# Performance work log

Measured on AMD Instinct MI355X. Metric: run time of the kernel, lower is better.

The kernel has to match this reference:

```python
import jax, jax.numpy as jnp
import numpy as np

NUM_KERNELS = 5


def setup_inputs() -> dict:
    key = jax.random.key(0)
    k1, k2 = jax.random.split(key)
    B, D = 4096, 256
    return {
        "s_feat": jax.random.normal(k1, (B, D), dtype=jnp.float32),
        "t_feat": jax.random.normal(k2, (B, D), dtype=jnp.float32),
    }


def _pairwise_sq_dists(feats):
    # Gram-matrix form of sum((x_i - x_j)**2, axis=-1); same math as the
    # broadcasted (x - y)**2 sum, without the [N, N, D] intermediate.
    sq = jnp.sum(feats * feats, axis=-1)  # [N]
    d = sq[:, None] + sq[None, :] - 2.0 * (feats @ feats.T)  # [N, N]
    return jnp.maximum(d, 0.0)


def reference(s_feat, t_feat):
    batch = s_feat.shape[0]
    feats = jnp.concatenate((s_feat, t_feat), axis=0)  # [2B, D]
    distances = _pairwise_sq_dists(feats)  # [2B, 2B]

    # Median-heuristic-style bandwidth (detached in original).
    n = 2 * batch
    bandwidth = float(n * n - n) / jnp.sum(jax.lax.stop_gradient(distances))
    bandwidth = bandwidth / (2 ** (NUM_KERNELS // 2))
    gammas = [bandwidth * (2 ** i) for i in range(NUM_KERNELS)]

    # Multi-gamma Gaussian kernel average (fixed small loop over kernels).
    kern = sum(jnp.exp(-distances * g) for g in gammas) / NUM_KERNELS

    s2s = kern[:batch, :batch]
    t2t = kern[batch:, batch:]
    s2t = kern[:batch, batch:]
    disc = jnp.mean(s2s + t2t - 2.0 * s2t)
    return disc
```

## Files before the change

kernel.cpp:

```cpp
#include <hip/hip_runtime.h>
#include <stdint.h>
#include <math.h>

#define BATCH 4096
#define NT    8192
#define FD    256
#define TM    256
#define TN    128
#define BK    32
#define NUMK  5
#define NBLK  1056
#define PBLK  1024

typedef __attribute__((ext_vector_type(8))) short bf16x8;
typedef __attribute__((ext_vector_type(4))) float f32x4;

static const size_t WS_FB    = 0;
static const size_t WS_SQ    = (size_t)NT * FD * 2;
static const size_t WS_PCOL  = WS_SQ + (size_t)NT * 4;
static const size_t WS_WSUM  = WS_PCOL + (size_t)PBLK * 256 * 4;
static const size_t WS_GAMMA = WS_WSUM + (size_t)PBLK * 4;

__device__ __forceinline__ unsigned short f2bf_rne(float x) {
    unsigned u = __float_as_uint(x);
    unsigned r = (u + 0x7fffu + ((u >> 16) & 1u)) >> 16;
    return (unsigned short)r;
}

__device__ __forceinline__ void async_copy16(void* lds, const void* g) {
    __builtin_amdgcn_global_load_lds(
        (__attribute__((address_space(1))) void*)(void*)(const_cast<void*>(g)),
        (__attribute__((address_space(3))) void*)lds, 16, 0, 0);
}

__global__ void mmd_prep(const float* __restrict__ s_feat,
                         const float* __restrict__ t_feat,
                         unsigned short* __restrict__ fb,
                         float* __restrict__ sq,
                         float* __restrict__ pcol,
                         float* __restrict__ wsum) {
    __shared__ float cp[4][FD];
    __shared__ float rw[4];
    const int w    = threadIdx.x >> 6;
    const int lane = threadIdx.x & 63;
    float c0 = 0.f, c1 = 0.f, c2 = 0.f, c3 = 0.f;
    float wtot = 0.f;
#pragma unroll
    for (int t = 0; t < 2; ++t) {
        int row = blockIdx.x * 8 + w * 2 + t;
        const float* src = (row < BATCH) ? (s_feat + (size_t)row * FD)
                                         : (t_feat + (size_t)(row - BATCH) * FD);
        float4 v = ((const float4*)src)[lane];
        unsigned int u01 = (unsigned)f2bf_rne(v.x) | ((unsigned)f2bf_rne(v.y) << 16);
        unsigned int u23 = (unsigned)f2bf_rne(v.z) | ((unsigned)f2bf_rne(v.w) << 16);
        ((uint2*)(fb + (size_t)row * FD))[lane] = make_uint2(u01, u23);
        float ss = v.x * v.x + v.y * v.y + v.z * v.z + v.w * v.w;
        for (int off = 32; off; off >>= 1) ss += __shfl_down(ss, off);
        if (lane == 0) { sq[row] = ss; wtot += ss; }
        c0 += v.x; c1 += v.y; c2 += v.z; c3 += v.w;
    }
    cp[w][4 * lane + 0] = c0;
    cp[w][4 * lane + 1] = c1;
    cp[w][4 * lane + 2] = c2;
    cp[w][4 * lane + 3] = c3;
    if (lane == 0) rw[w] = wtot;
    __syncthreads();
    int t = threadIdx.x;
    pcol[(size_t)blockIdx.x * 256 + t] = cp[0][t] + cp[1][t] + cp[2][t] + cp[3][t];
    if (t == 0) wsum[blockIdx.x] = rw[0] + rw[1] + rw[2] + rw[3];
}

__global__ void mmd_gamma(const float* __restrict__ pcol,
                          const float* __restrict__ wsum,
                          float* __restrict__ gamma,
                          float* __restrict__ out) {
    __shared__ float gcol[4][256];
    __shared__ float redc[4], redw[16];
    const int tid  = threadIdx.x;
    const int c    = tid & 255, s = tid >> 8;
    const int lane = tid & 63;
    float a0 = 0.f, a1 = 0.f, a2 = 0.f, a3 = 0.f;
#pragma unroll 4
    for (int k = 0; k < 256; k += 4) {
        a0 += pcol[(size_t)(s * 256 + k + 0) * 256 + c];
        a1 += pcol[(size_t)(s * 256 + k + 1) * 256 + c];
        a2 += pcol[(size_t)(s * 256 + k + 2) * 256 + c];
        a3 += pcol[(size_t)(s * 256 + k + 3) * 256 + c];
    }
    gcol[s][c] = (a0 + a1) + (a2 + a3);
    float wv = wsum[tid];
    for (int off = 32; off; off >>= 1) wv += __shfl_down(wv, off);
    if (lane == 0) redw[tid >> 6] = wv;
    __syncthreads();
    if (tid < 256) {
        float colv = gcol[0][c] + gcol[1][c] + gcol[2][c] + gcol[3][c];
        float cv2 = colv * colv;
        for (int off = 32; off; off >>= 1) cv2 += __shfl_down(cv2, off);
        if (lane == 0) redc[tid >> 6] = cv2;
    }
    __syncthreads();
    if (tid == 0) {
        float s2 = (redc[0] + redc[1]) + (redc[2] + redc[3]);
        float ssq = 0.f;
#pragma unroll
        for (int i = 0; i < 16; ++i) ssq += redw[i];
        float sumd = 2.0f * (float)NT * ssq - 2.0f * s2;
        float n2n  = (float)((long long)NT * NT - NT);
        gamma[0]   = 0.25f * (n2n / sumd);
        out[0]     = 0.f;
    }
}

__global__ __launch_bounds__(512, 4) void mmd_main(
    const unsigned short* __restrict__ fb,
    const float* __restrict__ sq,
    const float* __restrict__ gamma,
    float* __restrict__ out) {
    const int bid = blockIdx.x;
    const int swz = (bid & 7) * (NBLK / 8) + (bid >> 3);
    int I = (int)((65.0f - sqrtf(fmaxf(4225.0f - 4.0f * (float)swz, 0.f))) * 0.5f);
    if (I > 31) I = 31;
    while (I > 0 && I * (65 - I) > swz) --I;
    while (I < 31 && (I + 1) * (65 - (I + 1)) <= swz) ++I;
    const int J = 2 * I + (swz - I * (65 - I));
    const bool straddle = ((J >> 1) == I);

    __shared__ __align__(16) unsigned short a_t[3][TM * BK];
    __shared__ __align__(16) unsigned short b_t[3][TN * BK];
    __shared__ float sqa[TM], sqb[TN];
    __shared__ float red[8];

    const int tid  = threadIdx.x;
    const int w    = tid >> 6, lane = tid & 63;
    const int wm2  = w >> 1, wn2 = w & 1;
    const int quad = lane >> 4, m16 = lane & 15;
    const int lrow16 = lane >> 2;
    const int pslot  = lane & 3;

    const size_t rowA0 = (size_t)I * TM;
    const size_t rowB0 = (size_t)J * TN;

    float sqv = 0.f;
    if (tid < TM)                sqv = sq[rowA0 + tid];
    else if (tid < TM + TN)      sqv = sq[rowB0 + (tid - TM)];
    const float g0 = gamma[0];

#define STAGE(buf, k0_) do {                                                   \
        _Pragma("unroll")                                                      \
        for (int q = 0; q < 2; ++q) {                                          \
            int rr_ = w * 32 + q * 16 + lrow16;                    \
            int gc_ = pslot ^ ((rr_ >> 1) & 3);                                \
            async_copy16(&a_t[buf][(w * 32 + q * 16) * BK],                    \
                         fb + (rowA0 + rr_) * FD + (k0_) + gc_ * 8);           \
        }                                                                      \
        {                                                                      \
            int rr_ = w * 16 + lrow16;                             \
            int gc_ = pslot ^ ((rr_ >> 1) & 3);                                \
            async_copy16(&b_t[buf][(w * 16) * BK],                             \
                         fb + (rowB0 + rr_) * FD + (k0_) + gc_ * 8);           \
        }                                                                      \
    } while (0)

    STAGE(0, 0);
    STAGE(1, BK);
    STAGE(2, 2 * BK);

    if (tid < TM)                sqa[tid] = sqv;
    else if (tid < TM + TN)      sqb[tid - TM] = sqv;

    const f32x4 fzero = {0.f, 0.f, 0.f, 0.f};
    f32x4 acc[4][4];
#pragma unroll
    for (int a = 0; a < 4; ++a)
#pragma unroll
        for (int b = 0; b < 4; ++b) acc[a][b] = fzero;

    __syncthreads();

#pragma unroll
    for (int st = 0; st < 8; ++st) {
        if (st > 0) {
            if (st >= 3) {
                if (st == 7) asm volatile("s_waitcnt vmcnt(0)" ::: "memory");
                else         asm volatile("s_waitcnt vmcnt(3)" ::: "memory");
            }
            __builtin_amdgcn_s_barrier();
            __builtin_amdgcn_sched_barrier(0);
            if (st <= 5) STAGE((st + 2) % 3, (st + 2) * BK);
        }
        const int cur = st % 3;

        bf16x8 af[4], bf[4];
#pragma unroll
        for (int tm = 0; tm < 4; ++tm) {
            int row = wm2 * 64 + tm * 16 + m16;
            int p = quad ^ ((row >> 1) & 3);
            af[tm] = *(const bf16x8*)&a_t[cur][row * BK + p * 8];
        }
#pragma unroll
        for (int tn = 0; tn < 4; ++tn) {
            int row = wn2 * 64 + tn * 16 + m16;
            int p = quad ^ ((row >> 1) & 3);
            bf[tn] = *(const bf16x8*)&b_t[cur][row * BK + p * 8];
        }
        __builtin_amdgcn_sched_barrier(0);

        __builtin_amdgcn_s_setprio(1);
#pragma unroll
        for (int tm = 0; tm < 4; ++tm)
#pragma unroll
            for (int tn = 0; tn < 4; ++tn)
                acc[tm][tn] = __builtin_amdgcn_mfma_f32_16x16x32_bf16(
                    af[tm], bf[tn], acc[tm][tn], 0, 0, 0);
        __builtin_amdgcn_s_setprio(0);
    }

    float ls[4] = {0.f, 0.f, 0.f, 0.f};
    if (!straddle) {
#pragma unroll
        for (int tm = 0; tm < 4; ++tm) {
            const int i0 = wm2 * 64 + tm * 16 + quad * 4;
            float sqi[4] = {sqa[i0 + 0], sqa[i0 + 1], sqa[i0 + 2], sqa[i0 + 3]};
#pragma unroll
            for (int tn = 0; tn < 4; ++tn) {
                const int j = wn2 * 64 + tn * 16 + m16;
                const float sqj = sqb[j];
#pragma unroll
                for (int rr = 0; rr < 4; ++rr) {
                    float d = fmaf(-2.f, acc[tm][tn][rr], sqi[rr] + sqj);
                    d = fmaxf(d, 0.f);
                    float e1 = __expf(-d * g0);
                    float e2 = e1 * e1, e4 = e2 * e2, e8 = e4 * e4, e16 = e8 * e8;
                    ls[rr] += e1 + e2 + e4 + e8 + e16;
                }
            }
        }
    } else {
        const int dOff = (J - 2 * I) * TN;
#pragma unroll
        for (int tm = 0; tm < 4; ++tm) {
            const int i0 = wm2 * 64 + tm * 16 + quad * 4;
            float sqi[4] = {sqa[i0 + 0], sqa[i0 + 1], sqa[i0 + 2], sqa[i0 + 3]};
#pragma unroll
            for (int tn = 0; tn < 4; ++tn) {
                const int j = wn2 * 64 + tn * 16 + m16;
                const float sqj = sqb[j];
                const int jg = j + dOff;
#pragma unroll
                for (int rr = 0; rr < 4; ++rr) {
                    const int ig = i0 + rr;
                    float wf = (jg > ig) ? 2.f : ((jg == ig) ? 1.f : 0.f);
                    float d = fmaf(-2.f, acc[tm][tn][rr], sqi[rr] + sqj);
                    d = fmaxf(d, 0.f);
                    float e1 = __expf(-d * g0);
                    float e2 = e1 * e1, e4 = e2 * e2, e8 = e4 * e4, e16 = e8 * e8;
                    ls[rr] += wf * (e1 + e2 + e4 + e8 + e16);
                }
            }
        }
    }
    float lsum = (ls[0] + ls[1]) + (ls[2] + ls[3]);
    for (int off = 32; off; off >>= 1) lsum += __shfl_down(lsum, off);
    if (lane == 0) red[w] = lsum;
    __syncthreads();
    if (tid == 0) {
        float wgt;
        if (straddle) wgt = 1.f;
        else wgt = ((I < 16) == (J < 32)) ? 2.f : -2.f;
        float scale = wgt * (1.f / NUMK) * (1.f / 16777216.f);
        float tot = ((red[0] + red[1]) + (red[2] + red[3]))
                  + ((red[4] + red[5]) + (red[6] + red[7]));
        atomicAdd(out, tot * scale);
    }
}

extern "C" void kernel_launch(void* const* d_in, const int* in_sizes, int n_in,
                              void* d_out, int out_size, void* d_ws, size_t ws_size,
                              hipStream_t stream) {
    const float* s_feat = (const float*)d_in[0];
    const float* t_feat = (const float*)d_in[1];
    char* ws = (char*)d_ws;
    unsigned short* fb = (unsigned short*)(ws + WS_FB);
    float* sq    = (float*)(ws + WS_SQ);
    float* pcol  = (float*)(ws + WS_PCOL);
    float* wsum  = (float*)(ws + WS_WSUM);
    float* gamma = (float*)(ws + WS_GAMMA);
    float* out   = (float*)d_out;

    mmd_prep<<<PBLK, 256, 0, stream>>>(s_feat, t_feat, fb, sq, pcol, wsum);
    mmd_gamma<<<1, 1024, 0, stream>>>(pcol, wsum, gamma, out);
    mmd_main<<<NBLK, 512, 0, stream>>>(fb, sq, gamma, out);
}
```

Before: 108.1 us.

## Use square 128x128 triangular tiles with per-wave private LDS double buffers

Replaces the 256x128 rectangular tiling over the triangle (with straddle-tile masking) with 2080 square 128x128 upper-triangular tiles, each handled by a 256-thread block of four waves. Every wave now loads its own 64-row A and B slices into a private LDS double buffer, which removes the block-wide barriers in the K loop. Diagonal tiles are weighted once and off-diagonal tiles twice, so the per-element masking goes away. In exchange, each wave fetches its own copies with no sharing of A/B across waves, so global/L2 traffic per tile goes up and occupancy changes.

```diff
diff --git a/kernel.cpp b/kernel.cpp
--- a/kernel.cpp
+++ b/kernel.cpp
@@ -5,11 +5,10 @@
 #define BATCH 4096
 #define NT    8192
 #define FD    256
-#define TM    256
-#define TN    128
+#define TILE  128
 #define BK    32
 #define NUMK  5
-#define NBLK  1056
+#define NTRI  2080
 #define PBLK  1024
 
 typedef __attribute__((ext_vector_type(8))) short bf16x8;
@@ -111,62 +110,61 @@
     }
 }
 
-__global__ __launch_bounds__(512, 4) void mmd_main(
+__global__ __launch_bounds__(256, 2) void mmd_main(
     const unsigned short* __restrict__ fb,
     const float* __restrict__ sq,
     const float* __restrict__ gamma,
     float* __restrict__ out) {
     const int bid = blockIdx.x;
-    const int swz = (bid & 7) * (NBLK / 8) + (bid >> 3);
-    int I = (int)((65.0f - sqrtf(fmaxf(4225.0f - 4.0f * (float)swz, 0.f))) * 0.5f);
-    if (I > 31) I = 31;
-    while (I > 0 && I * (65 - I) > swz) --I;
-    while (I < 31 && (I + 1) * (65 - (I + 1)) <= swz) ++I;
-    const int J = 2 * I + (swz - I * (65 - I));
-    const bool straddle = ((J >> 1) == I);
-
-    __shared__ __align__(16) unsigned short a_t[3][TM * BK];
-    __shared__ __align__(16) unsigned short b_t[3][TN * BK];
-    __shared__ float sqa[TM], sqb[TN];
-    __shared__ float red[8];
+    const int swz = (bid & 7) * (NTRI / 8) + (bid >> 3);
+    int r = (int)((sqrtf(8.0f * (float)swz + 1.0f) - 1.0f) * 0.5f);
+    while ((r + 1) * (r + 2) / 2 <= swz) ++r;
+    while (r * (r + 1) / 2 > swz) --r;
+    const int bi = swz - r * (r + 1) / 2;
+    const int bj = r;
+
+    __shared__ __align__(16) unsigned short a_t[4][2][64 * BK];
+    __shared__ __align__(16) unsigned short b_t[4][2][64 * BK];
+    __shared__ float sqa[TILE], sqb[TILE];
+    __shared__ float red[4];
 
     const int tid  = threadIdx.x;
     const int w    = tid >> 6, lane = tid & 63;
-    const int wm2  = w >> 1, wn2 = w & 1;
+    const int wm   = w >> 1, wn = w & 1;
     const int quad = lane >> 4, m16 = lane & 15;
     const int lrow16 = lane >> 2;
     const int pslot  = lane & 3;
 
-    const size_t rowA0 = (size_t)I * TM;
-    const size_t rowB0 = (size_t)J * TN;
+    const size_t rowA0 = (size_t)bi * TILE + wm * 64;
+    const size_t rowB0 = (size_t)bj * TILE + wn * 64;
 
     float sqv = 0.f;
-    if (tid < TM)                sqv = sq[rowA0 + tid];
-    else if (tid < TM + TN)      sqv = sq[rowB0 + (tid - TM)];
+    if (tid < TILE) sqv = sq[(size_t)bi * TILE + tid];
+    else            sqv = sq[(size_t)bj * TILE + (tid - TILE)];
     const float g0 = gamma[0];
 
-#define STAGE(buf, k0_) do {                                                   \
+#define STAGE_W(buf, k0_) do {                                                 \
         _Pragma("unroll")                                                      \
-        for (int q = 0; q < 2; ++q) {                                          \
-            int rr_ = w * 32 + q * 16 + lrow16;                    \
+        for (int q = 0; q < 4; ++q) {                                          \
+            int rr_ = q * 16 + lrow16;                    \
             int gc_ = pslot ^ ((rr_ >> 1) & 3);                                \
-            async_copy16(&a_t[buf][(w * 32 + q * 16) * BK],                    \
+            async_copy16(&a_t[w][buf][(q * 16) * BK],                          \
                          fb + (rowA0 + rr_) * FD + (k0_) + gc_ * 8);           \
         }                                                                      \
-        {                                                                      \
-            int rr_ = w * 16 + lrow16;                             \
+        _Pragma("unroll")                                                      \
+        for (int q = 0; q < 4; ++q) {                                          \
+            int rr_ = q * 16 + lrow16;                                         \
             int gc_ = pslot ^ ((rr_ >> 1) & 3);                                \
-            async_copy16(&b_t[buf][(w * 16) * BK],                             \
+            async_copy16(&b_t[w][buf][(q * 16) * BK],                          \
                          fb + (rowB0 + rr_) * FD + (k0_) + gc_ * 8);           \
         }                                                                      \
     } while (0)
 
-    STAGE(0, 0);
-    STAGE(1, BK);
-    STAGE(2, 2 * BK);
-
-    if (tid < TM)                sqa[tid] = sqv;
-    else if (tid < TM + TN)      sqb[tid - TM] = sqv;
+    STAGE_W(0, 0);
+    STAGE_W(1, BK);
+
+    if (tid < TILE) sqa[tid] = sqv;
+    else            sqb[tid - TILE] = sqv;
 
     const f32x4 fzero = {0.f, 0.f, 0.f, 0.f};
     f32x4 acc[4][4];
@@ -175,34 +173,29 @@
 #pragma unroll
         for (int b = 0; b < 4; ++b) acc[a][b] = fzero;
 
-    __syncthreads();
-
 #pragma unroll
     for (int st = 0; st < 8; ++st) {
-        if (st > 0) {
-            if (st >= 3) {
-                if (st == 7) asm volatile("s_waitcnt vmcnt(0)" ::: "memory");
-                else         asm volatile("s_waitcnt vmcnt(3)" ::: "memory");
-            }
-            __builtin_amdgcn_s_barrier();
-            __builtin_amdgcn_sched_barrier(0);
-            if (st <= 5) STAGE((st + 2) % 3, (st + 2) * BK);
+        const int cur = st & 1;
+        if (st == 7) asm volatile("s_waitcnt vmcnt(0)" ::: "memory");
+        else         asm volatile("s_waitcnt vmcnt(8)" ::: "memory");
+        __builtin_amdgcn_sched_barrier(0);
+
+        bf16x8 af[4], bf[4];
+#pragma unroll
+        for (int tm = 0; tm < 4; ++tm) {
+            int ra = tm * 16 + m16;
+            int p = quad ^ ((ra >> 1) & 3);
+            af[tm] = *(const bf16x8*)&a_t[w][cur][ra * BK + p * 8];
         }
-        const int cur = st % 3;
-
-        bf16x8 af[4], bf[4];
-#pragma unroll
-        for (int tm = 0; tm < 4; ++tm) {
-            int row = wm2 * 64 + tm * 16 + m16;
-            int p = quad ^ ((row >> 1) & 3);
-            af[tm] = *(const bf16x8*)&a_t[cur][row * BK + p * 8];
+#pragma unroll
+        for (int tn = 0; tn < 4; ++tn) {
+            int rb = tn * 16 + m16;
+            int p = quad ^ ((rb >> 1) & 3);
+            bf[tn] = *(const bf16x8*)&b_t[w][cur][rb * BK + p * 8];
         }
-#pragma unroll
-        for (int tn = 0; tn < 4; ++tn) {
-            int row = wn2 * 64 + tn * 16 + m16;
-            int p = quad ^ ((row >> 1) & 3);
-            bf[tn] = *(const bf16x8*)&b_t[cur][row * BK + p * 8];
-        }
+        asm volatile("s_waitcnt lgkmcnt(0)" ::: "memory");
+        __builtin_amdgcn_sched_barrier(0);
+        if (st < 6) STAGE_W(cur, (st + 2) * BK);
         __builtin_amdgcn_sched_barrier(0);
 
         __builtin_amdgcn_s_setprio(1);
@@ -215,47 +208,24 @@
         __builtin_amdgcn_s_setprio(0);
     }
 
+    __syncthreads();
+
     float ls[4] = {0.f, 0.f, 0.f, 0.f};
-    if (!straddle) {
-#pragma unroll
-        for (int tm = 0; tm < 4; ++tm) {
-            const int i0 = wm2 * 64 + tm * 16 + quad * 4;
-            float sqi[4] = {sqa[i0 + 0], sqa[i0 + 1], sqa[i0 + 2], sqa[i0 + 3]};
-#pragma unroll
-            for (int tn = 0; tn < 4; ++tn) {
-                const int j = wn2 * 64 + tn * 16 + m16;
-                const float sqj = sqb[j];
-#pragma unroll
-                for (int rr = 0; rr < 4; ++rr) {
-                    float d = fmaf(-2.f, acc[tm][tn][rr], sqi[rr] + sqj);
-                    d = fmaxf(d, 0.f);
-                    float e1 = __expf(-d * g0);
-                    float e2 = e1 * e1, e4 = e2 * e2, e8 = e4 * e4, e16 = e8 * e8;
-                    ls[rr] += e1 + e2 + e4 + e8 + e16;
-                }
-            }
-        }
-    } else {
-        const int dOff = (J - 2 * I) * TN;
-#pragma unroll
-        for (int tm = 0; tm < 4; ++tm) {
-            const int i0 = wm2 * 64 + tm * 16 + quad * 4;
-            float sqi[4] = {sqa[i0 + 0], sqa[i0 + 1], sqa[i0 + 2], sqa[i0 + 3]};
-#pragma unroll
-            for (int tn = 0; tn < 4; ++tn) {
-                const int j = wn2 * 64 + tn * 16 + m16;
-                const float sqj = sqb[j];
-                const int jg = j + dOff;
-#pragma unroll
-                for (int rr = 0; rr < 4; ++rr) {
-                    const int ig = i0 + rr;
-                    float wf = (jg > ig) ? 2.f : ((jg == ig) ? 1.f : 0.f);
-                    float d = fmaf(-2.f, acc[tm][tn][rr], sqi[rr] + sqj);
-                    d = fmaxf(d, 0.f);
-                    float e1 = __expf(-d * g0);
-                    float e2 = e1 * e1, e4 = e2 * e2, e8 = e4 * e4, e16 = e8 * e8;
-                    ls[rr] += wf * (e1 + e2 + e4 + e8 + e16);
-                }
+#pragma unroll
+    for (int tm = 0; tm < 4; ++tm) {
+        const int i0 = wm * 64 + tm * 16 + quad * 4;
+        float sqi[4] = {sqa[i0 + 0], sqa[i0 + 1], sqa[i0 + 2], sqa[i0 + 3]};
+#pragma unroll
+        for (int tn = 0; tn < 4; ++tn) {
+            const int j = wn * 64 + tn * 16 + m16;
+            const float sqj = sqb[j];
+#pragma unroll
+            for (int rr = 0; rr < 4; ++rr) {
+                float d = fmaf(-2.f, acc[tm][tn][rr], sqi[rr] + sqj);
+                d = fmaxf(d, 0.f);
+                float e1 = __expf(-d * g0);
+                float e2 = e1 * e1, e4 = e2 * e2, e8 = e4 * e4, e16 = e8 * e8;
+                ls[rr] += e1 + e2 + e4 + e8 + e16;
             }
         }
     }
@@ -265,12 +235,10 @@
     __syncthreads();
     if (tid == 0) {
         float wgt;
-        if (straddle) wgt = 1.f;
-        else wgt = ((I < 16) == (J < 32)) ? 2.f : -2.f;
+        if (bi == bj) wgt = 1.f;
+        else wgt = ((bi < 32) == (bj < 32)) ? 2.f : -2.f;
         float scale = wgt * (1.f / NUMK) * (1.f / 16777216.f);
-        float tot = ((red[0] + red[1]) + (red[2] + red[3]))
-                  + ((red[4] + red[5]) + (red[6] + red[7]));
-        atomicAdd(out, tot * scale);
+        atomicAdd(out, (red[0] + red[1] + red[2] + red[3]) * scale);
     }
 }
 
@@ -289,5 +257,5 @@
 
     mmd_prep<<<PBLK, 256, 0, stream>>>(s_feat, t_feat, fb, sq, pcol, wsum);
     mmd_gamma<<<1, 1024, 0, stream>>>(pcol, wsum, gamma, out);
-    mmd_main<<<NBLK, 512, 0, stream>>>(fb, sq, gamma, out);
-}
+    mmd_main<<<NTRI, 256, 0, stream>>>(fb, sq, gamma, out);
+}
```

New measurement: 117.4 us. 1.09x slower.
